# Kernel optimization log

Measured on AMD Instinct MI355X. Metric: run time of the kernel, lower is better.

## Reference

```python
import jax, jax.numpy as jnp
import numpy as np

N = 96
M = 96
# visual field constants
L_V_EX, S_V_EX, L_V_IN, S_V_IN = 1.6, 3.5, 1.23, 6.3
FV, TAU_V, UPS_V, P_V, K_V = 1.0, 3.0, 3.0, 0.3, 7.0
# auditory field constants
L_A_EX, S_A_EX, L_A_IN, S_A_IN = 1.0, 5.3, 0.8, 11.8
FA, TAU_A, UPS_A, P_A, K_A = 1.0, 3.0, 3.0, 0.3, 3.0
# multisensory field constants
L_M_EX, S_M_EX, L_M_IN, S_M_IN = 3.8, 3.5, 3.3, 6.2
TAU_M, UPS_M, P_M = 3.0, 3.0, 0.3


def _torus_sqdist():
    # squared toroidal distance components: dx2[i,h], dy2[j,k]
    ii = jnp.arange(N, dtype=jnp.float32)
    jj = jnp.arange(M, dtype=jnp.float32)
    dx = jnp.abs(ii[:, None] - ii[None, :])
    dx = jnp.minimum(dx, N - dx)
    dy = jnp.abs(jj[:, None] - jj[None, :])
    dy = jnp.minimum(dy, M - dy)
    # aux[i,j,h,k] = dx[i,h]^2 + dy[j,k]^2
    return dx[:, None, :, None] ** 2 + dy[None, :, None, :] ** 2


def _dog(aux, l_ex, s_ex, l_in, s_in):
    # Faithful to source: exp(-aux/2 * sigma**2) == exp(-0.5*aux*sigma^2)
    return l_ex * jnp.exp(-0.5 * aux * (s_ex ** 2)) - l_in * jnp.exp(-0.5 * aux * (s_in ** 2))


def setup_inputs() -> dict:
    key = jax.random.key(0)
    ks = jax.random.split(key, 7)
    return {
        "video": jax.random.normal(ks[0], (32, 1024), dtype=jnp.float32),
        "audio": jax.random.normal(ks[1], (32, 2048), dtype=jnp.float32),
        "rf_v": jax.random.normal(ks[2], (N, M, 1024), dtype=jnp.float32) * (1.0 / np.sqrt(1024.0)),
        "rf_a": jax.random.normal(ks[3], (N, M, 2048), dtype=jnp.float32) * (1.0 / np.sqrt(2048.0)),
        "na_v": jax.random.normal(ks[4], (N, M), dtype=jnp.float32),
        "na_a": jax.random.normal(ks[5], (N, M), dtype=jnp.float32),
        "na_m": jax.random.normal(ks[6], (N, M), dtype=jnp.float32),
    }


def reference(video, audio, rf_v, rf_a, na_v, na_a, na_m):
    aux = _torus_sqdist()  # (N, M, N, M)
    syn_v = _dog(aux, L_V_EX, S_V_EX, L_V_IN, S_V_IN)
    syn_a = _dog(aux, L_A_EX, S_A_EX, L_A_IN, S_A_IN)
    syn_m = _dog(aux, L_M_EX, S_M_EX, L_M_IN, S_M_IN)

    # external inputs: sum over feature dim -> (B, N, M)
    ext_v = jnp.einsum('bv,ijv->bij', video, rf_v)
    ext_a = jnp.einsum('ba,ija->bij', audio, rf_a)

    # all-pairs neighbor inputs: neighbor[i,j] = sum_{h,k} act[h,k] * syn[i,j,h,k]
    nb_v = jnp.einsum('ijhk,hk->ij', syn_v, na_v)
    nb_a = jnp.einsum('ijhk,hk->ij', syn_a, na_a)

    coll_v = FV * na_m
    coll_a = FA * na_m

    na_v_new = na_v * (TAU_V - 1.0) / TAU_V + (1.0 / TAU_V) * jax.nn.sigmoid(
        (ext_v + nb_v - UPS_V + coll_v) * P_V)  # (B, N, M)
    na_a_new = na_a * (TAU_A - 1.0) / TAU_A + (1.0 / TAU_A) * jax.nn.sigmoid(
        (ext_a + nb_a - UPS_A + coll_a) * P_A)  # (B, N, M)

    nb_m = jnp.einsum('ijhk,hk->ij', syn_m, na_m)
    na_m_new = na_m * (TAU_M - 1.0) / TAU_M + (1.0 / TAU_M) * jax.nn.sigmoid(
        (K_V * na_v_new + K_A * na_a_new + nb_m - UPS_M) * P_M)  # (B, N, M)
    return na_m_new
```

## Files before the change

### kernel.cpp

```cpp
#include <hip/hip_runtime.h>
#include <math.h>

#define NN   96
#define NPOS (96*96)
#define BB   32
#define KV   1024
#define KA   2048

#define EXTV_OFF  0
#define EXTA0_OFF (BB*NPOS)
#define EXTA1_OFF (2*BB*NPOS)
#define CPT_OFF   (3*BB*NPOS)
#define AFV_OFF   (CPT_OFF + 6*NPOS)
#define AFV_SLOTS ((KV/32)*2*64)
#define AFA_OFF   (AFV_OFF + AFV_SLOTS*4)
#define AFA_SLOTS ((KA/32)*2*64)

typedef __bf16 bf16x8 __attribute__((ext_vector_type(8)));
typedef __bf16 bf16x4 __attribute__((ext_vector_type(4)));
typedef float  f32x4  __attribute__((ext_vector_type(4)));

__global__ __launch_bounds__(256) void nbT_kernel(
    const float* __restrict__ na_v, const float* __restrict__ na_a,
    const float* __restrict__ na_m, const float* __restrict__ video,
    const float* __restrict__ audio, float* __restrict__ ws)
{
    __shared__ float G[96][100];
    __shared__ float act_s[96][100];
    __shared__ float T1t[24][100];

    if (blockIdx.x >= 24) {
        const int e = (blockIdx.x - 24) * 256 + threadIdx.x;
        const float* src; bf16x8* dst; int K, el;
        if (e < AFV_SLOTS) { src = video; K = KV; dst = (bf16x8*)(ws + AFV_OFF); el = e; }
        else               { src = audio; K = KA; dst = (bf16x8*)(ws + AFA_OFF); el = e - AFV_SLOTS; }
        const int l  = el & 63;
        const int hb = (el >> 6) & 1;
        const int sg = el >> 7;
        const int b  = hb * 16 + (l & 15);
        const int k0 = sg * 32 + ((l >> 4) << 3);
        const float4 f0 = *(const float4*)&src[(size_t)b * K + k0];
        const float4 f1 = *(const float4*)&src[(size_t)b * K + k0 + 4];
        bf16x8 v;
        v[0] = (__bf16)f0.x; v[1] = (__bf16)f0.y; v[2] = (__bf16)f0.z; v[3] = (__bf16)f0.w;
        v[4] = (__bf16)f1.x; v[5] = (__bf16)f1.y; v[6] = (__bf16)f1.z; v[7] = (__bf16)f1.w;
        dst[el] = v;
        return;
    }

    const int c  = blockIdx.x >> 2;
    const int js = (blockIdx.x & 3) * 24;
    float l, s;
    if      (c == 0) { l =  1.60f; s = 3.5f;  }
    else if (c == 1) { l = -1.23f; s = 6.3f;  }
    else if (c == 2) { l =  1.00f; s = 5.3f;  }
    else if (c == 3) { l = -0.80f; s = 11.8f; }
    else if (c == 4) { l =  3.80f; s = 3.5f;  }
    else             { l = -3.30f; s = 6.2f;  }
    const float s2 = s * s;
    const int f = c >> 1;
    const float* act = (f == 0) ? na_v : (f == 1) ? na_a : na_m;
    const int tid = threadIdx.x;
    float* cpt = ws + CPT_OFF;

    for (int idx = tid; idx < 9216; idx += 256) {
        int j = idx / 96, k = idx - j * 96;
        int d = abs(j - k); d = min(d, 96 - d);
        G[j][k]     = __expf(-0.5f * (float)(d * d) * s2);
        act_s[j][k] = act[idx];
    }
    __syncthreads();

    const int hg3 = (tid >> 3) * 3;
    const int jl3 = (tid & 7) * 3;

    float t1[3][3] = {};
    for (int k0 = 0; k0 < 96; k0 += 4) {
        float4 av[3], gv[3];
        #pragma unroll
        for (int r = 0; r < 3; r++) {
            av[r] = *(const float4*)&act_s[hg3 + r][k0];
            gv[r] = *(const float4*)&G[js + jl3 + r][k0];
        }
        #pragma unroll
        for (int hh = 0; hh < 3; hh++)
            #pragma unroll
            for (int jj = 0; jj < 3; jj++)
                t1[hh][jj] += av[hh].x * gv[jj].x + av[hh].y * gv[jj].y
                            + av[hh].z * gv[jj].z + av[hh].w * gv[jj].w;
    }
    #pragma unroll
    for (int hh = 0; hh < 3; hh++)
        #pragma unroll
        for (int jj = 0; jj < 3; jj++)
            T1t[jl3 + jj][hg3 + hh] = t1[hh][jj];
    __syncthreads();

    float o[3][3] = {};
    for (int h0 = 0; h0 < 96; h0 += 4) {
        float4 gv[3], tv[3];
        #pragma unroll
        for (int r = 0; r < 3; r++) {
            gv[r] = *(const float4*)&G[hg3 + r][h0];
            tv[r] = *(const float4*)&T1t[jl3 + r][h0];
        }
        #pragma unroll
        for (int ii = 0; ii < 3; ii++)
            #pragma unroll
            for (int jj = 0; jj < 3; jj++)
                o[ii][jj] += gv[ii].x * tv[jj].x + gv[ii].y * tv[jj].y
                           + gv[ii].z * tv[jj].z + gv[ii].w * tv[jj].w;
    }
    #pragma unroll
    for (int ii = 0; ii < 3; ii++)
        #pragma unroll
        for (int jj = 0; jj < 3; jj++)
            cpt[c * NPOS + (hg3 + ii) * 96 + (js + jl3 + jj)] = l * o[ii][jj];
}

#define LDS_ROW 2064
__global__ __launch_bounds__(256, 4) void ext_mfma(
    const float* __restrict__ rf_v, const float* __restrict__ rf_a,
    float* __restrict__ ws)
{
    __shared__ char lds[16 * LDS_ROW + 2048];
    const int tid = threadIdx.x;
    const int bid = blockIdx.x;

    const float* rf; const bf16x8* af; float* ext; int K, kb, pt;
    if (bid < 1152) {
        const int c = bid / 576; pt = bid - c * 576;
        rf = rf_a; K = KA; kb = c << 10;
        af  = (const bf16x8*)(ws + AFA_OFF);
        ext = ws + EXTA0_OFF + c * (BB * NPOS);
    } else {
        pt = bid - 1152; rf = rf_v; K = KV; kb = 0;
        af  = (const bf16x8*)(ws + AFV_OFF);
        ext = ws + EXTV_OFF;
    }

    {
        const float* src = rf + (size_t)(pt * 16) * K + kb + tid * 4;
        float4 fa[8];
        #pragma unroll
        for (int j = 0; j < 8; ++j) fa[j] = *(const float4*)(src + (size_t)j * K);
        #pragma unroll
        for (int j = 0; j < 8; ++j) {
            bf16x4 v;
            v[0] = (__bf16)fa[j].x; v[1] = (__bf16)fa[j].y;
            v[2] = (__bf16)fa[j].z; v[3] = (__bf16)fa[j].w;
            *(bf16x4*)(lds + j * LDS_ROW + tid * 8) = v;
        }
        #pragma unroll
        for (int j = 0; j < 8; ++j) fa[j] = *(const float4*)(src + (size_t)(j + 8) * K);
        #pragma unroll
        for (int j = 0; j < 8; ++j) {
            bf16x4 v;
            v[0] = (__bf16)fa[j].x; v[1] = (__bf16)fa[j].y;
            v[2] = (__bf16)fa[j].z; v[3] = (__bf16)fa[j].w;
            *(bf16x4*)(lds + (j + 8) * LDS_ROW + tid * 8) = v;
        }
    }
    __syncthreads();

    const int l  = tid & 63, w = tid >> 6;
    const int bh = w & 1, kh = w >> 1;
    const bf16x8* ap = af + ((kb >> 5) + (kh << 4)) * 128 + (bh << 6) + l;
    const char*   bp = lds + (l & 15) * LDS_ROW + (kh << 10) + ((l >> 4) << 4);
    f32x4 acc = {0.f, 0.f, 0.f, 0.f};
    #pragma unroll
    for (int s = 0; s < 16; ++s) {
        bf16x8 a = ap[s * 128];
        bf16x8 b = *(const bf16x8*)(bp + s * 64);
        acc = __builtin_amdgcn_mfma_f32_16x16x32_bf16(a, b, acc, 0, 0, 0);
    }

    if (kh) *(f32x4*)(lds + 16 * LDS_ROW + (bh << 10) + l * 16) = acc;
    __syncthreads();
    if (!kh) {
        f32x4 o = *(const f32x4*)(lds + 16 * LDS_ROW + (bh << 10) + l * 16);
        acc += o;
        const int pcol = pt * 16 + (l & 15);
        const int br0  = (bh << 4) + ((l >> 4) << 2);
        #pragma unroll
        for (int r = 0; r < 4; ++r)
            ext[(size_t)(br0 + r) * NPOS + pcol] = acc[r];
    }
}

__global__ __launch_bounds__(256) void combine_kernel(
    const float* __restrict__ na_v, const float* __restrict__ na_a,
    const float* __restrict__ na_m, const float* __restrict__ ws,
    float* __restrict__ out)
{
    const int npq = NPOS >> 2;
    const int t = blockIdx.x * 256 + threadIdx.x;
    if (t >= BB * npq) return;
    const int b  = t / npq;
    const int p0 = (t - b * npq) << 2;

    float4 ev  = *(const float4*)&ws[EXTV_OFF  + (size_t)b * NPOS + p0];
    float4 ea0 = *(const float4*)&ws[EXTA0_OFF + (size_t)b * NPOS + p0];
    float4 ea1 = *(const float4*)&ws[EXTA1_OFF + (size_t)b * NPOS + p0];
    float4 ea = {ea0.x + ea1.x, ea0.y + ea1.y, ea0.z + ea1.z, ea0.w + ea1.w};
    const float* cpt = ws + CPT_OFF;
    float4 q0 = *(const float4*)&cpt[0 * NPOS + p0];
    float4 q1 = *(const float4*)&cpt[1 * NPOS + p0];
    float4 q2 = *(const float4*)&cpt[2 * NPOS + p0];
    float4 q3 = *(const float4*)&cpt[3 * NPOS + p0];
    float4 q4 = *(const float4*)&cpt[4 * NPOS + p0];
    float4 q5 = *(const float4*)&cpt[5 * NPOS + p0];
    float4 nv = *(const float4*)&na_v[p0];
    float4 na = *(const float4*)&na_a[p0];
    float4 nm = *(const float4*)&na_m[p0];

    float evs[4] = {ev.x, ev.y, ev.z, ev.w};
    float eas[4] = {ea.x, ea.y, ea.z, ea.w};
    float nbv[4] = {q0.x + q1.x, q0.y + q1.y, q0.z + q1.z, q0.w + q1.w};
    float nba[4] = {q2.x + q3.x, q2.y + q3.y, q2.z + q3.z, q2.w + q3.w};
    float nbm[4] = {q4.x + q5.x, q4.y + q5.y, q4.z + q5.z, q4.w + q5.w};
    float nvs[4] = {nv.x, nv.y, nv.z, nv.w};
    float nas[4] = {na.x, na.y, na.z, na.w};
    float nms[4] = {nm.x, nm.y, nm.z, nm.w};

    float4 o;
    float* os = (float*)&o;
    #pragma unroll
    for (int u = 0; u < 4; u++) {
        const float xv = (evs[u] + nbv[u] - 3.0f + nms[u]) * 0.3f;
        const float nav_new = nvs[u] * (2.f / 3.f) + (1.f / 3.f) / (1.f + __expf(-xv));
        const float xa = (eas[u] + nba[u] - 3.0f + nms[u]) * 0.3f;
        const float naa_new = nas[u] * (2.f / 3.f) + (1.f / 3.f) / (1.f + __expf(-xa));
        const float xm = (7.0f * nav_new + 3.0f * naa_new + nbm[u] - 3.0f) * 0.3f;
        os[u] = nms[u] * (2.f / 3.f) + (1.f / 3.f) / (1.f + __expf(-xm));
    }
    *(float4*)&out[(size_t)b * NPOS + p0] = o;
}

extern "C" void kernel_launch(void* const* d_in, const int* in_sizes, int n_in,
                              void* d_out, int out_size, void* d_ws, size_t ws_size,
                              hipStream_t stream) {
    const float* video = (const float*)d_in[0];
    const float* audio = (const float*)d_in[1];
    const float* rf_v  = (const float*)d_in[2];
    const float* rf_a  = (const float*)d_in[3];
    const float* na_v  = (const float*)d_in[4];
    const float* na_a  = (const float*)d_in[5];
    const float* na_m  = (const float*)d_in[6];
    float* ws  = (float*)d_ws;
    float* out = (float*)d_out;

    nbT_kernel<<<72, 256, 0, stream>>>(na_v, na_a, na_m, video, audio, ws);
    ext_mfma<<<1728, 256, 0, stream>>>(rf_v, rf_a, ws);
    combine_kernel<<<(BB * NPOS / 4 + 255) / 256, 256, 0, stream>>>(
        na_v, na_a, na_m, ws, out);
}
```

Measured before the change: 37.83 us.

## Pipeline ext MFMA kernel over K with double-buffered LDS and fewer blocks

Restructures the ext_mfma GEMV-like kernel so each block handles 32 positions over the full K range, looping over 256-wide K chunks with double-buffered LDS. Global loads for the next chunk overlap the MFMAs on the current one. Because the audio split-K and the cross-wave reduction are gone, one partial ext buffer and one add disappear from the combine kernel. In exchange the grid shrinks from 1728 to 576 blocks, and each block does a longer serial loop with more syncs, which may lower the memory parallelism available for streaming rf.

```diff
diff --git a/kernel.cpp b/kernel.cpp
--- a/kernel.cpp
+++ b/kernel.cpp
@@ -8,8 +8,7 @@
 #define KA   2048
 
 #define EXTV_OFF  0
-#define EXTA0_OFF (BB*NPOS)
-#define EXTA1_OFF (2*BB*NPOS)
+#define EXTA_OFF  (BB*NPOS)
 #define CPT_OFF   (3*BB*NPOS)
 #define AFV_OFF   (CPT_OFF + 6*NPOS)
 #define AFV_SLOTS ((KV/32)*2*64)
@@ -118,74 +117,103 @@
             cpt[c * NPOS + (hg3 + ii) * 96 + (js + jl3 + jj)] = l * o[ii][jj];
 }
 
-#define LDS_ROW 2064
+#define LROW 528
+#define BUFSZ (32*LROW)
 __global__ __launch_bounds__(256, 4) void ext_mfma(
     const float* __restrict__ rf_v, const float* __restrict__ rf_a,
     float* __restrict__ ws)
 {
-    __shared__ char lds[16 * LDS_ROW + 2048];
+    __shared__ char lds[2 * BUFSZ];
     const int tid = threadIdx.x;
     const int bid = blockIdx.x;
-
-    const float* rf; const bf16x8* af; float* ext; int K, kb, pt;
-    if (bid < 1152) {
-        const int c = bid / 576; pt = bid - c * 576;
-        rf = rf_a; K = KA; kb = c << 10;
-        af  = (const bf16x8*)(ws + AFA_OFF);
-        ext = ws + EXTA0_OFF + c * (BB * NPOS);
+    const int l = tid & 63, w = tid >> 6;
+
+    const float* rf; const bf16x8* af; float* ext; int K, NS, pt;
+    if (bid < 288) {
+        pt = bid; rf = rf_a; K = KA; NS = 8;
+        af = (const bf16x8*)(ws + AFA_OFF); ext = ws + EXTA_OFF;
     } else {
-        pt = bid - 1152; rf = rf_v; K = KV; kb = 0;
-        af  = (const bf16x8*)(ws + AFV_OFF);
-        ext = ws + EXTV_OFF;
-    }
-
-    {
-        const float* src = rf + (size_t)(pt * 16) * K + kb + tid * 4;
-        float4 fa[8];
-        #pragma unroll
-        for (int j = 0; j < 8; ++j) fa[j] = *(const float4*)(src + (size_t)j * K);
-        #pragma unroll
-        for (int j = 0; j < 8; ++j) {
-            bf16x4 v;
-            v[0] = (__bf16)fa[j].x; v[1] = (__bf16)fa[j].y;
-            v[2] = (__bf16)fa[j].z; v[3] = (__bf16)fa[j].w;
-            *(bf16x4*)(lds + j * LDS_ROW + tid * 8) = v;
-        }
-        #pragma unroll
-        for (int j = 0; j < 8; ++j) fa[j] = *(const float4*)(src + (size_t)(j + 8) * K);
-        #pragma unroll
-        for (int j = 0; j < 8; ++j) {
-            bf16x4 v;
-            v[0] = (__bf16)fa[j].x; v[1] = (__bf16)fa[j].y;
-            v[2] = (__bf16)fa[j].z; v[3] = (__bf16)fa[j].w;
-            *(bf16x4*)(lds + (j + 8) * LDS_ROW + tid * 8) = v;
-        }
-    }
+        pt = bid - 288; rf = rf_v; K = KV; NS = 4;
+        af = (const bf16x8*)(ws + AFV_OFF); ext = ws + EXTV_OFF;
+    }
+    const int p0 = pt * 32;
+
+    const float* src = rf + (size_t)(p0 + w) * K + l * 4;
+    const int bh = w & 1, ph = w >> 1;
+    const int row   = ph * 16 + (l & 15);
+    const int rboff = row * LROW + ((l >> 4) << 4);
+    const bf16x8* ap = af + (bh << 6) + l;
+
+    float4 fa[8];
+    bf16x8 av0, av1, av2, av3, av4, av5, av6, av7;
+    f32x4 acc = {0.f, 0.f, 0.f, 0.f};
+
+#define LOADS(S) do {                                                      \
+        _Pragma("unroll")                                                  \
+        for (int u = 0; u < 8; ++u)                                        \
+            fa[u] = *(const float4*)(src + (size_t)(4 * u) * K + (S) * 256); \
+    } while (0)
+
+#define WRITE(S) do {                                                      \
+        char* bw = lds + ((S) & 1) * BUFSZ + l * 8;                        \
+        _Pragma("unroll")                                                  \
+        for (int u = 0; u < 8; ++u) {                                      \
+            bf16x4 v;                                                      \
+            v[0] = (__bf16)fa[u].x; v[1] = (__bf16)fa[u].y;                \
+            v[2] = (__bf16)fa[u].z; v[3] = (__bf16)fa[u].w;                \
+            *(bf16x4*)(bw + (w + 4 * u) * LROW) = v;                       \
+        }                                                                  \
+    } while (0)
+
+#define AFLOAD(S) do {                                                     \
+        const bf16x8* a_ = ap + (size_t)(S) * 8 * 128;                     \
+        av0 = a_[0 * 128]; av1 = a_[1 * 128];                              \
+        av2 = a_[2 * 128]; av3 = a_[3 * 128];                              \
+        av4 = a_[4 * 128]; av5 = a_[5 * 128];                              \
+        av6 = a_[6 * 128]; av7 = a_[7 * 128];                              \
+    } while (0)
+
+#define COMP(S) do {                                                           \
+        const char* br = lds + ((S) & 1) * BUFSZ + rboff;                      \
+        bf16x8 b;                                                              \
+        b = *(const bf16x8*)(br + 0 * 64);                                     \
+        acc = __builtin_amdgcn_mfma_f32_16x16x32_bf16(av0, b, acc, 0, 0, 0);   \
+        b = *(const bf16x8*)(br + 1 * 64);                                     \
+        acc = __builtin_amdgcn_mfma_f32_16x16x32_bf16(av1, b, acc, 0, 0, 0);   \
+        b = *(const bf16x8*)(br + 2 * 64);                                     \
+        acc = __builtin_amdgcn_mfma_f32_16x16x32_bf16(av2, b, acc, 0, 0, 0);   \
+        b = *(const bf16x8*)(br + 3 * 64);                                     \
+        acc = __builtin_amdgcn_mfma_f32_16x16x32_bf16(av3, b, acc, 0, 0, 0);   \
+        b = *(const bf16x8*)(br + 4 * 64);                                     \
+        acc = __builtin_amdgcn_mfma_f32_16x16x32_bf16(av4, b, acc, 0, 0, 0);   \
+        b = *(const bf16x8*)(br + 5 * 64);                                     \
+        acc = __builtin_amdgcn_mfma_f32_16x16x32_bf16(av5, b, acc, 0, 0, 0);   \
+        b = *(const bf16x8*)(br + 6 * 64);                                     \
+        acc = __builtin_amdgcn_mfma_f32_16x16x32_bf16(av6, b, acc, 0, 0, 0);   \
+        b = *(const bf16x8*)(br + 7 * 64);                                     \
+        acc = __builtin_amdgcn_mfma_f32_16x16x32_bf16(av7, b, acc, 0, 0, 0);   \
+    } while (0)
+
+    LOADS(0); AFLOAD(0); WRITE(0);
     __syncthreads();
-
-    const int l  = tid & 63, w = tid >> 6;
-    const int bh = w & 1, kh = w >> 1;
-    const bf16x8* ap = af + ((kb >> 5) + (kh << 4)) * 128 + (bh << 6) + l;
-    const char*   bp = lds + (l & 15) * LDS_ROW + (kh << 10) + ((l >> 4) << 4);
-    f32x4 acc = {0.f, 0.f, 0.f, 0.f};
-    #pragma unroll
-    for (int s = 0; s < 16; ++s) {
-        bf16x8 a = ap[s * 128];
-        bf16x8 b = *(const bf16x8*)(bp + s * 64);
-        acc = __builtin_amdgcn_mfma_f32_16x16x32_bf16(a, b, acc, 0, 0, 0);
-    }
-
-    if (kh) *(f32x4*)(lds + 16 * LDS_ROW + (bh << 10) + l * 16) = acc;
-    __syncthreads();
-    if (!kh) {
-        f32x4 o = *(const f32x4*)(lds + 16 * LDS_ROW + (bh << 10) + l * 16);
-        acc += o;
-        const int pcol = pt * 16 + (l & 15);
-        const int br0  = (bh << 4) + ((l >> 4) << 2);
-        #pragma unroll
-        for (int r = 0; r < 4; ++r)
-            ext[(size_t)(br0 + r) * NPOS + pcol] = acc[r];
-    }
+    for (int s = 0; s < NS; ++s) {
+        const int nxt = s + 1;
+        if (nxt < NS) LOADS(nxt);
+        COMP(s);
+        if (nxt < NS) { AFLOAD(nxt); WRITE(nxt); }
+        __syncthreads();
+    }
+
+#undef LOADS
+#undef WRITE
+#undef AFLOAD
+#undef COMP
+
+    const int pcol = p0 + ph * 16 + (l & 15);
+    const int br0  = bh * 16 + ((l >> 4) << 2);
+    #pragma unroll
+    for (int r = 0; r < 4; ++r)
+        ext[(size_t)(br0 + r) * NPOS + pcol] = acc[r];
 }
 
 __global__ __launch_bounds__(256) void combine_kernel(
@@ -199,10 +227,8 @@
     const int b  = t / npq;
     const int p0 = (t - b * npq) << 2;
 
-    float4 ev  = *(const float4*)&ws[EXTV_OFF  + (size_t)b * NPOS + p0];
-    float4 ea0 = *(const float4*)&ws[EXTA0_OFF + (size_t)b * NPOS + p0];
-    float4 ea1 = *(const float4*)&ws[EXTA1_OFF + (size_t)b * NPOS + p0];
-    float4 ea = {ea0.x + ea1.x, ea0.y + ea1.y, ea0.z + ea1.z, ea0.w + ea1.w};
+    float4 ev = *(const float4*)&ws[EXTV_OFF + (size_t)b * NPOS + p0];
+    float4 ea = *(const float4*)&ws[EXTA_OFF + (size_t)b * NPOS + p0];
     const float* cpt = ws + CPT_OFF;
     float4 q0 = *(const float4*)&cpt[0 * NPOS + p0];
     float4 q1 = *(const float4*)&cpt[1 * NPOS + p0];
@@ -251,7 +277,7 @@
     float* out = (float*)d_out;
 
     nbT_kernel<<<72, 256, 0, stream>>>(na_v, na_a, na_m, video, audio, ws);
-    ext_mfma<<<1728, 256, 0, stream>>>(rf_v, rf_a, ws);
+    ext_mfma<<<576, 256, 0, stream>>>(rf_v, rf_a, ws);
     combine_kernel<<<(BB * NPOS / 4 + 255) / 256, 256, 0, stream>>>(
         na_v, na_a, na_m, ws, out);
 }
```

New measurement: 47.43 us. 25.4% more time.
